# Performance work log

Hardware: AMD Instinct MI355X
Metric: run time of the kernel (lower is better)

The kernel has to match this reference:

```python
import jax, jax.numpy as jnp
import numpy as np

B, XD, PD, D, H = 512, 32768, 512, 64, 128  # batch, x_dim, proj_dim, latent_dim, per_dim_hidden
G1 = 1024  # gene projector hidden (hardcoded in module)


def _init(k, shape, fan_in):
    s = 1.0 / np.sqrt(fan_in)
    return jax.random.uniform(k, shape, jnp.float32, -s, s)


def setup_inputs() -> dict:
    key = jax.random.key(0)
    ks = jax.random.split(key, 16)
    return {
        "x": jax.random.normal(ks[0], (B, XD), jnp.float32),
        "z": jax.random.normal(ks[1], (B, D), jnp.float32),
        "perm": jax.random.permutation(ks[2], B).astype(jnp.int32),
        # shared gene projector
        "Wg1": _init(ks[3], (XD, G1), XD), "bg1": _init(ks[4], (G1,), XD),
        "Wg2": _init(ks[5], (G1, PD), G1), "bg2": _init(ks[6], (PD,), G1),
        # per-dimension 3-layer MLPs, stacked over D. Layer-1 weight [PD+1, H]
        # is split into the h-part Wh and the z-part Wz (last input column).
        "Wh": _init(ks[7], (D, PD, H), PD + 1),
        "Wz": _init(ks[8], (D, H), PD + 1),
        "b1": _init(ks[9], (D, H), PD + 1),
        "W2": _init(ks[10], (D, H, H), H), "b2": _init(ks[11], (D, H), H),
        "W3": _init(ks[12], (D, H), H), "b3": _init(ks[13], (D,), H),
    }


def reference(x, z, perm, Wg1, bg1, Wg2, bg2, Wh, Wz, b1, W2, b2, W3, b3):
    elu = jax.nn.elu
    # shared gene projector (eval mode: dropout = identity, no noise)
    h = elu(elu(x @ Wg1 + bg1) @ Wg2 + bg2)            # [B, PD]
    # batched layer-1 of all D per-dim nets; h-projection computed once and
    # reused for the marginal pass via permutation (h_shuffled = h[perm]).
    hWh = jnp.einsum('bp,dph->bdh', h, Wh)             # [B, D, H]
    zWz = z[:, :, None] * Wz[None]                     # [B, D, H]

    def head(a1_pre):
        a1 = elu(a1_pre)                               # [B, D, H]
        a2 = elu(jnp.einsum('bdh,dhk->bdk', a1, W2) + b2)
        return jnp.einsum('bdh,dh->bd', a2, W3) + b3   # [B, D] scalar scores

    joint_score = head(hWh + zWz + b1)                 # T(h, z_j)
    marg_score = head(hWh[perm] + zWz + b1)            # T(h_shuffled, z_j)

    emas = jnp.ones((D,), x.dtype)                     # buffer init = ones, eval: no update
    et = jnp.mean(jnp.exp(marg_score), axis=0)         # [D]
    mi = jnp.mean(joint_score, axis=0) - jnp.log(et / emas)
    return -jnp.mean(mi)
```

## Files before the change

kernel.cpp:

```cpp
#include <hip/hip_runtime.h>
#include <hip/hip_bf16.h>
#include <math.h>

#define B_  512
#define XD_ 32768
#define PD_ 512
#define D_  64
#define H_  128
#define G1_ 1024

typedef __attribute__((ext_vector_type(8))) short short8v;
typedef __attribute__((ext_vector_type(4))) float floatx4;

__device__ __forceinline__ float eluf(float v) { return v > 0.f ? v : expm1f(v); }

__device__ __forceinline__ void split8t(const float* c, short8v& h, short8v& l) {
    unsigned hu[8], lu[8];
    #pragma unroll
    for (int j = 0; j < 8; j++) {
        unsigned u = __float_as_uint(c[j]);
        hu[j] = u & 0xFFFF0000u;
        float res = c[j] - __uint_as_float(hu[j]);
        lu[j] = __float_as_uint(res);
    }
    uint4 hp, lp;
    hp.x = __builtin_amdgcn_perm(hu[1], hu[0], 0x07060302u);
    hp.y = __builtin_amdgcn_perm(hu[3], hu[2], 0x07060302u);
    hp.z = __builtin_amdgcn_perm(hu[5], hu[4], 0x07060302u);
    hp.w = __builtin_amdgcn_perm(hu[7], hu[6], 0x07060302u);
    lp.x = __builtin_amdgcn_perm(lu[1], lu[0], 0x07060302u);
    lp.y = __builtin_amdgcn_perm(lu[3], lu[2], 0x07060302u);
    lp.z = __builtin_amdgcn_perm(lu[5], lu[4], 0x07060302u);
    lp.w = __builtin_amdgcn_perm(lu[7], lu[6], 0x07060302u);
    h = __builtin_bit_cast(short8v, hp);
    l = __builtin_bit_cast(short8v, lp);
}

__global__ __launch_bounds__(256) void k_trs(const float* __restrict__ x,
                                             ushort* __restrict__ xh,
                                             ushort* __restrict__ xl) {
    const int k0 = blockIdx.x * 64;
    const int m0 = blockIdx.y * 64;
    const int t = threadIdx.x;
    const int m = t & 63;
    const int kq = t >> 6;
    #pragma unroll
    for (int i = 0; i < 2; i++) {
        int kg = kq * 2 + i;
        const float* p = x + (size_t)(m0 + m) * XD_ + k0 + kg * 8;
        float4 v0 = *(const float4*)p, v1 = *(const float4*)(p + 4);
        float c[8] = {v0.x, v0.y, v0.z, v0.w, v1.x, v1.y, v1.z, v1.w};
        short8v h, l; split8t(c, h, l);
        size_t off = ((size_t)((k0 >> 3) + kg) * B_ + m0 + m) * 8;
        *(short8v*)(xh + off) = h;
        *(short8v*)(xl + off) = l;
    }
}

__global__ __launch_bounds__(256, 2) void k_gemm1t(const ushort* __restrict__ xh,
                                                   const ushort* __restrict__ xl,
                                                   const float* __restrict__ Wg1,
                                                   float* __restrict__ part,
                                                   int KS) {
    __shared__ ushort Ah[2][4 * 128 * 8], Al[2][4 * 128 * 8];
    __shared__ ushort Bh[2][4 * 128 * 8], Bl[2][4 * 128 * 8];
    const int nt = blockIdx.x, mt = blockIdx.y, ks = blockIdx.z;
    const int t = threadIdx.x;
    const int w = t >> 6, lane = t & 63;
    const int q = lane >> 4, l15 = lane & 15;
    const int wr = w >> 1, wc = w & 1;
    const int q4 = t >> 6, pr = t & 63;
    const int k0 = ks * KS;

    const size_t aoff = (((size_t)(k0 >> 3) + q4) * B_ + mt * 128 + pr) * 8;
    const ushort* Agh = xh + aoff;
    const ushort* Agl = xl + aoff;
    const float*  Bg  = Wg1 + (size_t)(k0 + q4 * 8) * G1_ + nt * 128 + pr * 2;

    floatx4 acc[4][4];
    #pragma unroll
    for (int i = 0; i < 4; i++)
        #pragma unroll
        for (int j = 0; j < 4; j++) acc[i][j] = (floatx4){0.f, 0.f, 0.f, 0.f};

    uint4 pAh0, pAh1, pAl0, pAl1;
    float2 pb[8];

    auto loadT = [&](int kt) {
        size_t o = (size_t)kt * B_;
        pAh0 = *(const uint4*)(Agh + o);
        pAh1 = *(const uint4*)(Agh + o + 512);
        pAl0 = *(const uint4*)(Agl + o);
        pAl1 = *(const uint4*)(Agl + o + 512);
        const float* p = Bg + (size_t)kt * G1_;
        #pragma unroll
        for (int kk = 0; kk < 8; kk++) pb[kk] = *(const float2*)(p + (size_t)kk * G1_);
    };

    auto stage = [&](int buf) {
        float c0[8], c1[8];
        #pragma unroll
        for (int kk = 0; kk < 8; kk++) { c0[kk] = pb[kk].x; c1[kk] = pb[kk].y; }
        short8v bh0, bl0, bh1, bl1;
        split8t(c0, bh0, bl0); split8t(c1, bh1, bl1);
        int n0 = pr * 2;
        int i0 = (q4 * 128 + (n0 ^ q4)) * 8;
        int i1 = (q4 * 128 + ((n0 + 1) ^ q4)) * 8;
        *(short8v*)&Bh[buf][i0] = bh0; *(short8v*)&Bl[buf][i0] = bl0;
        *(short8v*)&Bh[buf][i1] = bh1; *(short8v*)&Bl[buf][i1] = bl1;
        int ia0 = (q4 * 128 + (pr ^ q4)) * 8;
        *(uint4*)&Ah[buf][ia0] = pAh0;
        *(uint4*)&Al[buf][ia0] = pAl0;
        *(uint4*)&Ah[buf][ia0 + 512] = pAh1;
        *(uint4*)&Al[buf][ia0 + 512] = pAl1;
    };

    auto mma = [&](int buf) {
        short8v af[4], alf[4], bf[4], blf[4];
        #pragma unroll
        for (int i = 0; i < 4; i++) {
            int m = wr * 64 + i * 16 + l15;
            int idx = (q * 128 + (m ^ q)) * 8;
            af[i]  = *(const short8v*)&Ah[buf][idx];
            alf[i] = *(const short8v*)&Al[buf][idx];
        }
        #pragma unroll
        for (int j = 0; j < 4; j++) {
            int n = wc * 64 + j * 16 + l15;
            int idx = (q * 128 + (n ^ q)) * 8;
            bf[j]  = *(const short8v*)&Bh[buf][idx];
            blf[j] = *(const short8v*)&Bl[buf][idx];
        }
        #pragma unroll
        for (int i = 0; i < 4; i++)
            #pragma unroll
            for (int j = 0; j < 4; j++) {
                acc[i][j] = __builtin_amdgcn_mfma_f32_16x16x32_bf16(af[i],  bf[j],  acc[i][j], 0, 0, 0);
                acc[i][j] = __builtin_amdgcn_mfma_f32_16x16x32_bf16(af[i],  blf[j], acc[i][j], 0, 0, 0);
                acc[i][j] = __builtin_amdgcn_mfma_f32_16x16x32_bf16(alf[i], bf[j],  acc[i][j], 0, 0, 0);
            }
    };

    loadT(0);
    stage(0);
    loadT(32);
    asm volatile("s_waitcnt lgkmcnt(0)" ::: "memory");
    __builtin_amdgcn_s_barrier();

    const int NT = KS >> 5;
    for (int it = 0; it < NT - 1; it++) {
        const int cur = it & 1;
        stage(cur ^ 1);
        if (it + 2 < NT) loadT((it + 2) * 32);
        mma(cur);
        asm volatile("s_waitcnt lgkmcnt(0)" ::: "memory");
        __builtin_amdgcn_s_barrier();
    }
    mma((NT - 1) & 1);

    float* P = part + (size_t)ks * (B_ * G1_) + (size_t)(mt * 128) * G1_ + nt * 128;
    #pragma unroll
    for (int i = 0; i < 4; i++)
        #pragma unroll
        for (int j = 0; j < 4; j++) {
            int col = wc * 64 + j * 16 + l15;
            #pragma unroll
            for (int r = 0; r < 4; r++) {
                int row = wr * 64 + i * 16 + q * 4 + r;
                P[(size_t)row * G1_ + col] = acc[i][j][r];
            }
        }
}

__global__ __launch_bounds__(256, 2) void k_gemm1m(const float* __restrict__ x,
                                                   const float* __restrict__ Wg1,
                                                   float* __restrict__ part,
                                                   int KS) {
    __shared__ ushort Ah[4 * 128 * 8], Al[4 * 128 * 8];
    __shared__ ushort Bh[4 * 128 * 8], Bl[4 * 128 * 8];
    const int nt = blockIdx.x, mt = blockIdx.y, ks = blockIdx.z;
    const int t = threadIdx.x;
    const int w = t >> 6, lane = t & 63;
    const int q = lane >> 4, l15 = lane & 15;
    const int wr = w >> 1, wc = w & 1;
    const int kbB = t >> 6, nb = t & 63;
    const int mA = t & 127, kbA = t >> 7;
    const int k0 = ks * KS;

    const float* Ag = x + (size_t)(mt * 128 + mA) * XD_ + k0 + kbA * 8;
    const float* Bg = Wg1 + (size_t)(k0 + kbB * 8) * G1_ + nt * 128 + nb * 2;

    floatx4 acc[4][4];
    #pragma unroll
    for (int i = 0; i < 4; i++)
        #pragma unroll
        for (int j = 0; j < 4; j++) acc[i][j] = (floatx4){0.f, 0.f, 0.f, 0.f};

    float4 pa0 = *(const float4*)(Ag);
    float4 pa1 = *(const float4*)(Ag + 4);
    float4 pa2 = *(const float4*)(Ag + 16);
    float4 pa3 = *(const float4*)(Ag + 20);
    float2 pb[8];
    #pragma unroll
    for (int kk = 0; kk < 8; kk++) pb[kk] = *(const float2*)(Bg + (size_t)kk * G1_);

    for (int kt = 0; kt < KS; kt += 32) {
        float cA0[8] = {pa0.x, pa0.y, pa0.z, pa0.w, pa1.x, pa1.y, pa1.z, pa1.w};
        float cA1[8] = {pa2.x, pa2.y, pa2.z, pa2.w, pa3.x, pa3.y, pa3.z, pa3.w};
        float c0[8], c1[8];
        #pragma unroll
        for (int kk = 0; kk < 8; kk++) { c0[kk] = pb[kk].x; c1[kk] = pb[kk].y; }
        short8v ah0, al0, ah1, al1, bh0, bl0, bh1, bl1;
        split8t(cA0, ah0, al0);
        split8t(cA1, ah1, al1);
        split8t(c0, bh0, bl0);
        split8t(c1, bh1, bl1);
        if (kt + 32 < KS) {
            pa0 = *(const float4*)(Ag + kt + 32);
            pa1 = *(const float4*)(Ag + kt + 36);
            pa2 = *(const float4*)(Ag + kt + 48);
            pa3 = *(const float4*)(Ag + kt + 52);
            const float* p = Bg + (size_t)(kt + 32) * G1_;
            #pragma unroll
            for (int kk = 0; kk < 8; kk++) pb[kk] = *(const float2*)(p + (size_t)kk * G1_);
        }
        {
            int ia0 = (kbA * 128 + (mA ^ kbA)) * 8;
            int ia1 = ((kbA + 2) * 128 + (mA ^ (kbA + 2))) * 8;
            *(short8v*)&Ah[ia0] = ah0; *(short8v*)&Al[ia0] = al0;
            *(short8v*)&Ah[ia1] = ah1; *(short8v*)&Al[ia1] = al1;
            int n0i = nb * 2;
            int i0 = (kbB * 128 + (n0i ^ kbB)) * 8;
            int i1 = (kbB * 128 + ((n0i + 1) ^ kbB)) * 8;
            *(short8v*)&Bh[i0] = bh0; *(short8v*)&Bl[i0] = bl0;
            *(short8v*)&Bh[i1] = bh1; *(short8v*)&Bl[i1] = bl1;
        }
        __syncthreads();
        short8v af[4], alf[4], bf[4], blf[4];
        #pragma unroll
        for (int i = 0; i < 4; i++) {
            int m = wr * 64 + i * 16 + l15;
            int idx = (q * 128 + (m ^ q)) * 8;
            af[i]  = *(const short8v*)&Ah[idx];
            alf[i] = *(const short8v*)&Al[idx];
        }
        #pragma unroll
        for (int j = 0; j < 4; j++) {
            int n = wc * 64 + j * 16 + l15;
            int idx = (q * 128 + (n ^ q)) * 8;
            bf[j]  = *(const short8v*)&Bh[idx];
            blf[j] = *(const short8v*)&Bl[idx];
        }
        #pragma unroll
        for (int i = 0; i < 4; i++)
            #pragma unroll
            for (int j = 0; j < 4; j++) {
                acc[i][j] = __builtin_amdgcn_mfma_f32_16x16x32_bf16(af[i],  bf[j],  acc[i][j], 0, 0, 0);
                acc[i][j] = __builtin_amdgcn_mfma_f32_16x16x32_bf16(af[i],  blf[j], acc[i][j], 0, 0, 0);
                acc[i][j] = __builtin_amdgcn_mfma_f32_16x16x32_bf16(alf[i], bf[j],  acc[i][j], 0, 0, 0);
            }
        __syncthreads();
    }
    float* P = part + (size_t)ks * (B_ * G1_) + (size_t)(mt * 128) * G1_ + nt * 128;
    #pragma unroll
    for (int i = 0; i < 4; i++)
        #pragma unroll
        for (int j = 0; j < 4; j++) {
            int col = wc * 64 + j * 16 + l15;
            #pragma unroll
            for (int r = 0; r < 4; r++) {
                int row = wr * 64 + i * 16 + q * 4 + r;
                P[(size_t)row * G1_ + col] = acc[i][j][r];
            }
        }
}

__global__ __launch_bounds__(256) void k_red1(const float* __restrict__ part,
                                              const float* __restrict__ bg1,
                                              ushort* __restrict__ Gh,
                                              ushort* __restrict__ Gl,
                                              int nparts) {
    int idx = (blockIdx.x * 256 + threadIdx.x) * 8;
    const int S = B_ * G1_;
    float c[8] = {};
    for (int k = 0; k < nparts; k++) {
        const float* p = part + (size_t)k * S + idx;
        float4 v0 = *(const float4*)p, v1 = *(const float4*)(p + 4);
        c[0] += v0.x; c[1] += v0.y; c[2] += v0.z; c[3] += v0.w;
        c[4] += v1.x; c[5] += v1.y; c[6] += v1.z; c[7] += v1.w;
    }
    int cb = idx & (G1_ - 1);
    float4 b0 = *(const float4*)(bg1 + cb), b1v = *(const float4*)(bg1 + cb + 4);
    c[0] = eluf(c[0] + b0.x); c[1] = eluf(c[1] + b0.y);
    c[2] = eluf(c[2] + b0.z); c[3] = eluf(c[3] + b0.w);
    c[4] = eluf(c[4] + b1v.x); c[5] = eluf(c[5] + b1v.y);
    c[6] = eluf(c[6] + b1v.z); c[7] = eluf(c[7] + b1v.w);
    short8v h, l; split8t(c, h, l);
    *(short8v*)(Gh + idx) = h;
    *(short8v*)(Gl + idx) = l;
}

__global__ __launch_bounds__(256, 2) void k_gemm2m(const ushort* __restrict__ Gh,
                                                   const ushort* __restrict__ Gl,
                                                   const float* __restrict__ Wg2,
                                                   float* __restrict__ part2) {
    __shared__ ushort Ah[4 * 64 * 8], Al[4 * 64 * 8];
    __shared__ ushort Bh[4 * 64 * 8], Bl[4 * 64 * 8];
    const int nt = blockIdx.x, mt = blockIdx.y, ks = blockIdx.z;
    const int t = threadIdx.x;
    const int w = t >> 6, lane = t & 63;
    const int q = lane >> 4, l15 = lane & 15;
    const int kb = (t >> 4) & 3;
    const int rb = (t & 15) | (w << 4);
    const int k0 = ks * 128;

    const int cB = t & 63, g = t >> 6;

    floatx4 acc[4];
    #pragma unroll
    for (int i = 0; i < 4; i++) acc[i] = (floatx4){0.f, 0.f, 0.f, 0.f};

    for (int kt = 0; kt < 128; kt += 32) {
        {
            const ushort* pH = Gh + (size_t)(mt * 64 + rb) * G1_ + k0 + kt + kb * 8;
            const ushort* pL = Gl + (size_t)(mt * 64 + rb) * G1_ + k0 + kt + kb * 8;
            uint4 vh = *(const uint4*)pH;
            uint4 vl = *(const uint4*)pL;
            int idx = (kb * 64 + (rb ^ kb)) * 8;
            *(uint4*)&Ah[idx] = vh;
            *(uint4*)&Al[idx] = vl;
        }
        {
            float c[8];
            const float* p = Wg2 + (size_t)(k0 + kt + g * 8) * PD_ + nt * 64 + cB;
            #pragma unroll
            for (int kk = 0; kk < 8; kk++) c[kk] = p[(size_t)kk * PD_];
            short8v h, l; split8t(c, h, l);
            int idx = (g * 64 + (cB ^ g)) * 8;
            *(short8v*)&Bh[idx] = h;
            *(short8v*)&Bl[idx] = l;
        }
        __syncthreads();
        short8v af[4], alf[4], bf, blf;
        #pragma unroll
        for (int i = 0; i < 4; i++) {
            int m = i * 16 + l15;
            int idx = (q * 64 + (m ^ q)) * 8;
            af[i]  = *(const short8v*)&Ah[idx];
            alf[i] = *(const short8v*)&Al[idx];
        }
        {
            int n = w * 16 + l15;
            int idx = (q * 64 + (n ^ q)) * 8;
            bf  = *(const short8v*)&Bh[idx];
            blf = *(const short8v*)&Bl[idx];
        }
        #pragma unroll
        for (int i = 0; i < 4; i++) {
            acc[i] = __builtin_amdgcn_mfma_f32_16x16x32_bf16(af[i],  bf,  acc[i], 0, 0, 0);
            acc[i] = __builtin_amdgcn_mfma_f32_16x16x32_bf16(af[i],  blf, acc[i], 0, 0, 0);
            acc[i] = __builtin_amdgcn_mfma_f32_16x16x32_bf16(alf[i], bf,  acc[i], 0, 0, 0);
        }
        __syncthreads();
    }
    float* P = part2 + (size_t)ks * (B_ * PD_) + (size_t)(mt * 64) * PD_ + nt * 64;
    #pragma unroll
    for (int i = 0; i < 4; i++) {
        int col = w * 16 + l15;
        #pragma unroll
        for (int r = 0; r < 4; r++) {
            int row = i * 16 + q * 4 + r;
            P[(size_t)row * PD_ + col] = acc[i][r];
        }
    }
}

__global__ __launch_bounds__(256) void k_red2(const float* __restrict__ part2,
                                              const float* __restrict__ bg2,
                                              ushort* __restrict__ hh,
                                              ushort* __restrict__ hl) {
    int idx = (blockIdx.x * 256 + threadIdx.x) * 8;
    const int S = B_ * PD_;
    float c[8] = {};
    #pragma unroll
    for (int k = 0; k < 8; k++) {
        const float* p = part2 + (size_t)k * S + idx;
        float4 v0 = *(const float4*)p, v1 = *(const float4*)(p + 4);
        c[0] += v0.x; c[1] += v0.y; c[2] += v0.z; c[3] += v0.w;
        c[4] += v1.x; c[5] += v1.y; c[6] += v1.z; c[7] += v1.w;
    }
    int cb = idx & (PD_ - 1);
    float4 b0 = *(const float4*)(bg2 + cb), b1v = *(const float4*)(bg2 + cb + 4);
    c[0] = eluf(c[0] + b0.x); c[1] = eluf(c[1] + b0.y);
    c[2] = eluf(c[2] + b0.z); c[3] = eluf(c[3] + b0.w);
    c[4] = eluf(c[4] + b1v.x); c[5] = eluf(c[5] + b1v.y);
    c[6] = eluf(c[6] + b1v.z); c[7] = eluf(c[7] + b1v.w);
    short8v h, l; split8t(c, h, l);
    *(short8v*)(hh + idx) = h;
    *(short8v*)(hl + idx) = l;
}

__global__ __launch_bounds__(256, 2) void k_hwh_m(const ushort* __restrict__ hh,
                                                  const ushort* __restrict__ hl,
                                                  const float* __restrict__ Wh,
                                                  float* __restrict__ hWh) {
    __shared__ ushort Ah[4 * 64 * 8], Al[4 * 64 * 8];
    __shared__ ushort Bh[4 * 128 * 8], Bl[4 * 128 * 8];
    const int d = blockIdx.x, mt = blockIdx.y;
    const int t = threadIdx.x;
    const int w = t >> 6, lane = t & 63;
    const int q = lane >> 4, l15 = lane & 15;
    const int kb = (t >> 4) & 3;
    const int rb = (t & 15) | (w << 4);

    const ushort* AgH = hh + (size_t)(mt * 64 + rb) * PD_ + kb * 8;
    const ushort* AgL = hl + (size_t)(mt * 64 + rb) * PD_ + kb * 8;
    const float* Bg = Wh + (size_t)d * (PD_ * H_) + (size_t)(kb * 8) * H_ + rb * 2;

    floatx4 acc[4][2];
    #pragma unroll
    for (int i = 0; i < 4; i++)
        #pragma unroll
        for (int j = 0; j < 2; j++) acc[i][j] = (floatx4){0.f, 0.f, 0.f, 0.f};

    uint4 pah = *(const uint4*)(AgH);
    uint4 pal = *(const uint4*)(AgL);
    float2 pb[8];
    #pragma unroll
    for (int kk = 0; kk < 8; kk++) pb[kk] = *(const float2*)(Bg + (size_t)kk * H_);

    for (int kt = 0; kt < PD_; kt += 32) {
        float c0[8], c1[8];
        #pragma unroll
        for (int kk = 0; kk < 8; kk++) { c0[kk] = pb[kk].x; c1[kk] = pb[kk].y; }
        short8v bh0, bl0, bh1, bl1;
        split8t(c0, bh0, bl0);
        split8t(c1, bh1, bl1);
        uint4 ah = pah, al = pal;
        if (kt + 32 < PD_) {
            pah = *(const uint4*)(AgH + kt + 32);
            pal = *(const uint4*)(AgL + kt + 32);
            const float* p = Bg + (size_t)(kt + 32) * H_;
            #pragma unroll
            for (int kk = 0; kk < 8; kk++) pb[kk] = *(const float2*)(p + (size_t)kk * H_);
        }
        {
            int idx = (kb * 64 + (rb ^ kb)) * 8;
            *(uint4*)&Ah[idx] = ah;
            *(uint4*)&Al[idx] = al;
            int n0i = rb * 2;
            int i0 = (kb * 128 + (n0i ^ kb)) * 8;
            int i1 = (kb * 128 + ((n0i + 1) ^ kb)) * 8;
            *(short8v*)&Bh[i0] = bh0; *(short8v*)&Bl[i0] = bl0;
            *(short8v*)&Bh[i1] = bh1; *(short8v*)&Bl[i1] = bl1;
        }
        __syncthreads();
        short8v af[4], alf[4], bf[2], blf[2];
        #pragma unroll
        for (int i = 0; i < 4; i++) {
            int m = i * 16 + l15;
            int idx = (q * 64 + (m ^ q)) * 8;
            af[i]  = *(const short8v*)&Ah[idx];
            alf[i] = *(const short8v*)&Al[idx];
        }
        #pragma unroll
        for (int j = 0; j < 2; j++) {
            int n = w * 32 + j * 16 + l15;
            int idx = (q * 128 + (n ^ q)) * 8;
            bf[j]  = *(const short8v*)&Bh[idx];
            blf[j] = *(const short8v*)&Bl[idx];
        }
        #pragma unroll
        for (int i = 0; i < 4; i++)
            #pragma unroll
            for (int j = 0; j < 2; j++) {
                acc[i][j] = __builtin_amdgcn_mfma_f32_16x16x32_bf16(af[i],  bf[j],  acc[i][j], 0, 0, 0);
                acc[i][j] = __builtin_amdgcn_mfma_f32_16x16x32_bf16(af[i],  blf[j], acc[i][j], 0, 0, 0);
                acc[i][j] = __builtin_amdgcn_mfma_f32_16x16x32_bf16(alf[i], bf[j],  acc[i][j], 0, 0, 0);
            }
        __syncthreads();
    }
    #pragma unroll
    for (int i = 0; i < 4; i++)
        #pragma unroll
        for (int j = 0; j < 2; j++) {
            int col = w * 32 + j * 16 + l15;
            #pragma unroll
            for (int r = 0; r < 4; r++) {
                int row = i * 16 + q * 4 + r;
                int b = mt * 64 + row;
                hWh[(size_t)b * (D_ * H_) + d * H_ + col] = acc[i][j][r];
            }
        }
}

__global__ __launch_bounds__(256, 2) void k_heads(const float* __restrict__ hWh,
                                                  const float* __restrict__ z,
                                                  const int* __restrict__ perm,
                                                  const float* __restrict__ Wz,
                                                  const float* __restrict__ b1,
                                                  const float* __restrict__ W2,
                                                  const float* __restrict__ b2,
                                                  const float* __restrict__ W3,
                                                  const float* __restrict__ b3,
                                                  float* __restrict__ jpart,
                                                  float* __restrict__ epart) {
    const int chunk = blockIdx.x;
    const int d = blockIdx.y;
    const int pass = blockIdx.z;
    const int t = threadIdx.x;
    const int b0 = chunk * 64;
    __shared__ ushort A1h[16 * 64 * 8];
    __shared__ ushort A1l[16 * 64 * 8];
    __shared__ float  BS[4096];
    ushort* Bh = (ushort*)BS;
    ushort* Bl = Bh + 4096;
    float*  sred = BS;

    const int w = t >> 6, lane = t & 63;
    const int q = lane >> 4, l15 = lane & 15;
    const int kb = (t >> 4) & 3;
    const int rb = (t & 15) | (w << 4);

    const float* W2d = W2 + (size_t)d * H_ * H_;
    const float* Wzd = Wz + d * H_;
    const float* b1d = b1 + d * H_;
    const float* b2d = b2 + d * H_;
    const float* W3d = W3 + d * H_;

    {
        int i = t >> 2;
        int kt = t & 3;
        int h0 = kt * 32;
        int bb = b0 + i;
        int src = (pass == 0) ? bb : perm[bb];
        float zv = z[bb * D_ + d];
        const float* hrow = hWh + (size_t)src * (D_ * H_) + d * H_;
        #pragma unroll
        for (int kq = 0; kq < 4; kq++) {
            float c[8];
            int kbase = h0 + kq * 8;
            float4 v0 = *(const float4*)(hrow + kbase);
            float4 v1 = *(const float4*)(hrow + kbase + 4);
            float4 w0 = *(const float4*)(Wzd + kbase);
            float4 w1 = *(const float4*)(Wzd + kbase + 4);
            float4 x0 = *(const float4*)(b1d + kbase);
            float4 x1 = *(const float4*)(b1d + kbase + 4);
            c[0] = eluf(v0.x + zv * w0.x + x0.x);
            c[1] = eluf(v0.y + zv * w0.y + x0.y);
            c[2] = eluf(v0.z + zv * w0.z + x0.z);
            c[3] = eluf(v0.w + zv * w0.w + x0.w);
            c[4] = eluf(v1.x + zv * w1.x + x1.x);
            c[5] = eluf(v1.y + zv * w1.y + x1.y);
            c[6] = eluf(v1.z + zv * w1.z + x1.z);
            c[7] = eluf(v1.w + zv * w1.w + x1.w);
            short8v hv, lv; split8t(c, hv, lv);
            int idx = ((kt * 4 + kq) * 64 + (i ^ kq)) * 8;
            *(short8v*)&A1h[idx] = hv;
            *(short8v*)&A1l[idx] = lv;
        }
    }
    __syncthreads();
    floatx4 acc[4][2];
    #pragma unroll
    for (int i = 0; i < 4; i++)
        #pragma unroll
        for (int j = 0; j < 2; j++) acc[i][j] = (floatx4){0.f, 0.f, 0.f, 0.f};
    for (int kt2 = 0; kt2 < 4; kt2++) {
        {
            float c0[8], c1[8];
            const float* p = W2d + (size_t)(kt2 * 32 + kb * 8) * H_ + rb * 2;
            #pragma unroll
            for (int kk = 0; kk < 8; kk++) {
                float2 v = *(const float2*)(p + (size_t)kk * H_);
                c0[kk] = v.x; c1[kk] = v.y;
            }
            short8v h0v, l0v, h1v, l1v;
            split8t(c0, h0v, l0v);
            split8t(c1, h1v, l1v);
            int n0i = rb * 2;
            int i0 = (kb * 128 + (n0i ^ kb)) * 8;
            int i1 = (kb * 128 + ((n0i + 1) ^ kb)) * 8;
            *(short8v*)&Bh[i0] = h0v; *(short8v*)&Bl[i0] = l0v;
            *(short8v*)&Bh[i1] = h1v; *(short8v*)&Bl[i1] = l1v;
        }
        __syncthreads();
        short8v af[4], alf[4], bf[2], blf[2];
        #pragma unroll
        for (int i = 0; i < 4; i++) {
            int m = i * 16 + l15;
            int idx = ((kt2 * 4 + q) * 64 + (m ^ q)) * 8;
            af[i]  = *(const short8v*)&A1h[idx];
            alf[i] = *(const short8v*)&A1l[idx];
        }
        #pragma unroll
        for (int j = 0; j < 2; j++) {
            int n = w * 32 + j * 16 + l15;
            int idx = (q * 128 + (n ^ q)) * 8;
            bf[j]  = *(const short8v*)&Bh[idx];
            blf[j] = *(const short8v*)&Bl[idx];
        }
        #pragma unroll
        for (int i = 0; i < 4; i++)
            #pragma unroll
            for (int j = 0; j < 2; j++) {
                acc[i][j] = __builtin_amdgcn_mfma_f32_16x16x32_bf16(af[i],  bf[j],  acc[i][j], 0, 0, 0);
                acc[i][j] = __builtin_amdgcn_mfma_f32_16x16x32_bf16(af[i],  blf[j], acc[i][j], 0, 0, 0);
                acc[i][j] = __builtin_amdgcn_mfma_f32_16x16x32_bf16(alf[i], bf[j],  acc[i][j], 0, 0, 0);
            }
        __syncthreads();
    }
    #pragma unroll
    for (int i = 0; i < 4; i++) {
        #pragma unroll
        for (int r = 0; r < 4; r++) {
            int b = i * 16 + q * 4 + r;
            float s = 0.f;
            #pragma unroll
            for (int j = 0; j < 2; j++) {
                int col = w * 32 + j * 16 + l15;
                float a2v = eluf(acc[i][j][r] + b2d[col]);
                s = fmaf(a2v, W3d[col], s);
            }
            sred[b * 64 + w * 16 + l15] = s;
        }
    }
    __syncthreads();
    float val = 0.f;
    if (t < 64) {
        float s = b3[d];
        const float4* row = (const float4*)&sred[t * 64];
        #pragma unroll
        for (int c = 0; c < 16; c++) {
            float4 v = row[c];
            s += v.x + v.y + v.z + v.w;
        }
        val = (pass == 0) ? s : expf(s);
        #pragma unroll
        for (int off = 32; off > 0; off >>= 1)
            val += __shfl_down(val, off, 64);
    }
    if (t == 0) {
        if (pass == 0) jpart[d * 8 + chunk] = val;
        else           epart[d * 8 + chunk] = val;
    }
}

__global__ void k_final(const float* __restrict__ jpart,
                        const float* __restrict__ epart,
                        float* __restrict__ out) {
    int t = threadIdx.x;
    float mj = 0.f, me = 0.f;
    #pragma unroll
    for (int c = 0; c < 8; c++) { mj += jpart[t * 8 + c]; me += epart[t * 8 + c]; }
    mj *= (1.f / 512.f);
    me *= (1.f / 512.f);
    float mi = mj - logf(me);
    #pragma unroll
    for (int off = 32; off > 0; off >>= 1) mi += __shfl_down(mi, off, 64);
    if (t == 0) out[0] = -mi * (1.f / 64.f);
}

extern "C" void kernel_launch(void* const* d_in, const int* in_sizes, int n_in,
                              void* d_out, int out_size, void* d_ws, size_t ws_size,
                              hipStream_t stream) {
    const float* x   = (const float*)d_in[0];
    const float* z   = (const float*)d_in[1];
    const int*  perm = (const int*)d_in[2];
    const float* Wg1 = (const float*)d_in[3];
    const float* bg1 = (const float*)d_in[4];
    const float* Wg2 = (const float*)d_in[5];
    const float* bg2 = (const float*)d_in[6];
    const float* Wh  = (const float*)d_in[7];
    const float* Wz  = (const float*)d_in[8];
    const float* b1  = (const float*)d_in[9];
    const float* W2  = (const float*)d_in[10];
    const float* b2  = (const float*)d_in[11];
    const float* W3  = (const float*)d_in[12];
    const float* b3  = (const float*)d_in[13];
    float* out = (float*)d_out;

    char* base = (char*)d_ws;
    const size_t PART_SLICE = (size_t)B_ * G1_ * sizeof(float);

    const size_t NEW_NEED = 16 * PART_SLICE + 67108864ull + 2097152 + 1048576 + 4096;

    if (ws_size >= NEW_NEED) {
        float* part  = (float*)base;
        ushort* xh   = (ushort*)(base + 33554432);
        ushort* xl   = (ushort*)(base + 67108864);
        float* hWh   = (float*)base;
        float* part2 = (float*)(base + 16777216);
        ushort* Gh   = (ushort*)(base + 100663296);
        ushort* Gl   = Gh + 524288;
        ushort* hh   = (ushort*)(base + 102760448);
        ushort* hl   = hh + 262144;
        float* jpart = (float*)(base + 103809024);
        float* epart = jpart + 512;

        k_trs<<<dim3(512, 8), 256, 0, stream>>>(x, xh, xl);
        k_gemm1t<<<dim3(8, 4, 16), 256, 0, stream>>>(xh, xl, Wg1, part, XD_ / 16);
        k_red1<<<256, 256, 0, stream>>>(part, bg1, Gh, Gl, 16);
        k_gemm2m<<<dim3(8, 8, 8), 256, 0, stream>>>(Gh, Gl, Wg2, part2);
        k_red2<<<128, 256, 0, stream>>>(part2, bg2, hh, hl);
        k_hwh_m<<<dim3(64, 8), 256, 0, stream>>>(hh, hl, Wh, hWh);
        k_heads<<<dim3(8, 64, 2), 256, 0, stream>>>(hWh, z, perm, Wz, b1, W2, b2, W3, b3,
                                                    jpart, epart);
        k_final<<<1, 64, 0, stream>>>(jpart, epart, out);
    } else {
        int nks = (ws_size >= (size_t)32 * PART_SLICE + 3145728 + 4096) ? 32 : 16;
        const int KS = XD_ / nks;
        const size_t partBytes = (size_t)nks * PART_SLICE;

        float* part  = (float*)base;
        float* hWh   = (float*)base;
        float* part2 = (float*)(base + 16777216);
        ushort* Gh   = (ushort*)(base + partBytes);
        ushort* Gl   = Gh + 524288;
        ushort* hh   = (ushort*)(base + partBytes + 2097152);
        ushort* hl   = hh + 262144;
        float* jpart = (float*)(base + partBytes + 3145728);
        float* epart = jpart + 512;

        k_gemm1m<<<dim3(8, 4, nks), 256, 0, stream>>>(x, Wg1, part, KS);
        k_red1<<<256, 256, 0, stream>>>(part, bg1, Gh, Gl, nks);
        k_gemm2m<<<dim3(8, 8, 8), 256, 0, stream>>>(Gh, Gl, Wg2, part2);
        k_red2<<<128, 256, 0, stream>>>(part2, bg2, hh, hl);
        k_hwh_m<<<dim3(64, 8), 256, 0, stream>>>(hh, hl, Wh, hWh);
        k_heads<<<dim3(8, 64, 2), 256, 0, stream>>>(hWh, z, perm, Wz, b1, W2, b2, W3, b3,
                                                    jpart, epart);
        k_final<<<1, 64, 0, stream>>>(jpart, epart, out);
    }
}
```

Measured before the change: 427.8 us.

## Widen gemm1 to 512 threads with deeper K tile, fold head passes into one block

The main projector GEMM now runs 512-thread blocks that stage 64 K-elements per iteration, with 8 waves tiled 4x2 over a 128x128 output. It also halves the split-K count from 16 to 8, which reduces the partial-sum traffic that the reduction kernel must read, and raises MFMA issue priority with s_setprio. The heads kernel loops over the joint and marginal passes inside one block instead of launching a separate z-dimension per pass, so W2 staging and launch work are shared. The cost is fewer blocks in gemm1 (256 instead of 512), which may lower occupancy and latency hiding, and longer serial work per heads block.

After: 428.3 us. Within noise of the previous version (+0.1%).

```diff
diff --git a/kernel.cpp b/kernel.cpp
--- a/kernel.cpp
+++ b/kernel.cpp
@@ -57,42 +57,42 @@
     }
 }
 
-__global__ __launch_bounds__(256, 2) void k_gemm1t(const ushort* __restrict__ xh,
+__global__ __launch_bounds__(512, 2) void k_gemm1t(const ushort* __restrict__ xh,
                                                    const ushort* __restrict__ xl,
                                                    const float* __restrict__ Wg1,
                                                    float* __restrict__ part,
                                                    int KS) {
-    __shared__ ushort Ah[2][4 * 128 * 8], Al[2][4 * 128 * 8];
-    __shared__ ushort Bh[2][4 * 128 * 8], Bl[2][4 * 128 * 8];
+    __shared__ ushort Ah[2][8 * 128 * 8], Al[2][8 * 128 * 8];
+    __shared__ ushort Bh[2][8 * 128 * 8], Bl[2][8 * 128 * 8];
     const int nt = blockIdx.x, mt = blockIdx.y, ks = blockIdx.z;
     const int t = threadIdx.x;
     const int w = t >> 6, lane = t & 63;
     const int q = lane >> 4, l15 = lane & 15;
-    const int wr = w >> 1, wc = w & 1;
-    const int q4 = t >> 6, pr = t & 63;
+    const int wm = w & 3, wn = w >> 2;
+    const int kg = t >> 6, pr = t & 63;
     const int k0 = ks * KS;
 
-    const size_t aoff = (((size_t)(k0 >> 3) + q4) * B_ + mt * 128 + pr) * 8;
+    const size_t aoff = (((size_t)(k0 >> 3) + kg) * B_ + mt * 128 + pr) * 8;
     const ushort* Agh = xh + aoff;
     const ushort* Agl = xl + aoff;
-    const float*  Bg  = Wg1 + (size_t)(k0 + q4 * 8) * G1_ + nt * 128 + pr * 2;
-
-    floatx4 acc[4][4];
-    #pragma unroll
-    for (int i = 0; i < 4; i++)
+    const float*  Bg  = Wg1 + (size_t)(k0 + kg * 8) * G1_ + nt * 128 + pr * 2;
+
+    floatx4 acc[2][4];
+    #pragma unroll
+    for (int i = 0; i < 2; i++)
         #pragma unroll
         for (int j = 0; j < 4; j++) acc[i][j] = (floatx4){0.f, 0.f, 0.f, 0.f};
 
     uint4 pAh0, pAh1, pAl0, pAl1;
     float2 pb[8];
 
-    auto loadT = [&](int kt) {
-        size_t o = (size_t)kt * B_;
+    auto loadT = [&](int T) {
+        size_t o = (size_t)T * B_ * 64;
         pAh0 = *(const uint4*)(Agh + o);
         pAh1 = *(const uint4*)(Agh + o + 512);
         pAl0 = *(const uint4*)(Agl + o);
         pAl1 = *(const uint4*)(Agl + o + 512);
-        const float* p = Bg + (size_t)kt * G1_;
+        const float* p = Bg + (size_t)T * 64 * G1_;
         #pragma unroll
         for (int kk = 0; kk < 8; kk++) pb[kk] = *(const float2*)(p + (size_t)kk * G1_);
     };
@@ -104,54 +104,60 @@
         short8v bh0, bl0, bh1, bl1;
         split8t(c0, bh0, bl0); split8t(c1, bh1, bl1);
         int n0 = pr * 2;
-        int i0 = (q4 * 128 + (n0 ^ q4)) * 8;
-        int i1 = (q4 * 128 + ((n0 + 1) ^ q4)) * 8;
+        int i0 = (kg * 128 + (n0 ^ kg)) * 8;
+        int i1 = (kg * 128 + ((n0 + 1) ^ kg)) * 8;
         *(short8v*)&Bh[buf][i0] = bh0; *(short8v*)&Bl[buf][i0] = bl0;
         *(short8v*)&Bh[buf][i1] = bh1; *(short8v*)&Bl[buf][i1] = bl1;
-        int ia0 = (q4 * 128 + (pr ^ q4)) * 8;
-        *(uint4*)&Ah[buf][ia0] = pAh0;
-        *(uint4*)&Al[buf][ia0] = pAl0;
-        *(uint4*)&Ah[buf][ia0 + 512] = pAh1;
-        *(uint4*)&Al[buf][ia0 + 512] = pAl1;
+        int ia = (kg * 128 + (pr ^ kg)) * 8;
+        *(uint4*)&Ah[buf][ia] = pAh0;
+        *(uint4*)&Al[buf][ia] = pAl0;
+        *(uint4*)&Ah[buf][ia + 512] = pAh1;
+        *(uint4*)&Al[buf][ia + 512] = pAl1;
     };
 
     auto mma = [&](int buf) {
-        short8v af[4], alf[4], bf[4], blf[4];
-        #pragma unroll
-        for (int i = 0; i < 4; i++) {
-            int m = wr * 64 + i * 16 + l15;
-            int idx = (q * 128 + (m ^ q)) * 8;
-            af[i]  = *(const short8v*)&Ah[buf][idx];
-            alf[i] = *(const short8v*)&Al[buf][idx];
-        }
-        #pragma unroll
-        for (int j = 0; j < 4; j++) {
-            int n = wc * 64 + j * 16 + l15;
-            int idx = (q * 128 + (n ^ q)) * 8;
-            bf[j]  = *(const short8v*)&Bh[buf][idx];
-            blf[j] = *(const short8v*)&Bl[buf][idx];
-        }
-        #pragma unroll
-        for (int i = 0; i < 4; i++)
+        #pragma unroll
+        for (int s = 0; s < 2; s++) {
+            const int kgq = s * 4 + q;
+            short8v af[2], alf[2], bf[4], blf[4];
+            #pragma unroll
+            for (int i = 0; i < 2; i++) {
+                int m = wm * 32 + i * 16 + l15;
+                int idx = (kgq * 128 + (m ^ kgq)) * 8;
+                af[i]  = *(const short8v*)&Ah[buf][idx];
+                alf[i] = *(const short8v*)&Al[buf][idx];
+            }
             #pragma unroll
             for (int j = 0; j < 4; j++) {
-                acc[i][j] = __builtin_amdgcn_mfma_f32_16x16x32_bf16(af[i],  bf[j],  acc[i][j], 0, 0, 0);
-                acc[i][j] = __builtin_amdgcn_mfma_f32_16x16x32_bf16(af[i],  blf[j], acc[i][j], 0, 0, 0);
-                acc[i][j] = __builtin_amdgcn_mfma_f32_16x16x32_bf16(alf[i], bf[j],  acc[i][j], 0, 0, 0);
-            }
+                int n = wn * 64 + j * 16 + l15;
+                int idx = (kgq * 128 + (n ^ kgq)) * 8;
+                bf[j]  = *(const short8v*)&Bh[buf][idx];
+                blf[j] = *(const short8v*)&Bl[buf][idx];
+            }
+            __builtin_amdgcn_s_setprio(1);
+            #pragma unroll
+            for (int i = 0; i < 2; i++)
+                #pragma unroll
+                for (int j = 0; j < 4; j++) {
+                    acc[i][j] = __builtin_amdgcn_mfma_f32_16x16x32_bf16(af[i],  bf[j],  acc[i][j], 0, 0, 0);
+                    acc[i][j] = __builtin_amdgcn_mfma_f32_16x16x32_bf16(af[i],  blf[j], acc[i][j], 0, 0, 0);
+                    acc[i][j] = __builtin_amdgcn_mfma_f32_16x16x32_bf16(alf[i], bf[j],  acc[i][j], 0, 0, 0);
+                }
+            __builtin_amdgcn_s_setprio(0);
+        }
     };
 
     loadT(0);
     stage(0);
-    loadT(32);
+    loadT(1);
     asm volatile("s_waitcnt lgkmcnt(0)" ::: "memory");
     __builtin_amdgcn_s_barrier();
 
-    const int NT = KS >> 5;
+    const int NT = KS >> 6;
     for (int it = 0; it < NT - 1; it++) {
         const int cur = it & 1;
         stage(cur ^ 1);
-        if (it + 2 < NT) loadT((it + 2) * 32);
+        if (it + 2 < NT) loadT(it + 2);
         mma(cur);
         asm volatile("s_waitcnt lgkmcnt(0)" ::: "memory");
         __builtin_amdgcn_s_barrier();
@@ -160,13 +166,13 @@
 
     float* P = part + (size_t)ks * (B_ * G1_) + (size_t)(mt * 128) * G1_ + nt * 128;
     #pragma unroll
-    for (int i = 0; i < 4; i++)
+    for (int i = 0; i < 2; i++)
         #pragma unroll
         for (int j = 0; j < 4; j++) {
-            int col = wc * 64 + j * 16 + l15;
+            int col = wn * 64 + j * 16 + l15;
             #pragma unroll
             for (int r = 0; r < 4; r++) {
-                int row = wr * 64 + i * 16 + q * 4 + r;
+                int row = wm * 32 + i * 16 + q * 4 + r;
                 P[(size_t)row * G1_ + col] = acc[i][j][r];
             }
         }
@@ -507,7 +513,6 @@
                                                   float* __restrict__ epart) {
     const int chunk = blockIdx.x;
     const int d = blockIdx.y;
-    const int pass = blockIdx.z;
     const int t = threadIdx.x;
     const int b0 = chunk * 64;
     __shared__ ushort A1h[16 * 64 * 8];
@@ -528,121 +533,126 @@
     const float* b2d = b2 + d * H_;
     const float* W3d = W3 + d * H_;
 
-    {
-        int i = t >> 2;
-        int kt = t & 3;
-        int h0 = kt * 32;
-        int bb = b0 + i;
-        int src = (pass == 0) ? bb : perm[bb];
-        float zv = z[bb * D_ + d];
-        const float* hrow = hWh + (size_t)src * (D_ * H_) + d * H_;
-        #pragma unroll
-        for (int kq = 0; kq < 4; kq++) {
-            float c[8];
-            int kbase = h0 + kq * 8;
-            float4 v0 = *(const float4*)(hrow + kbase);
-            float4 v1 = *(const float4*)(hrow + kbase + 4);
-            float4 w0 = *(const float4*)(Wzd + kbase);
-            float4 w1 = *(const float4*)(Wzd + kbase + 4);
-            float4 x0 = *(const float4*)(b1d + kbase);
-            float4 x1 = *(const float4*)(b1d + kbase + 4);
-            c[0] = eluf(v0.x + zv * w0.x + x0.x);
-            c[1] = eluf(v0.y + zv * w0.y + x0.y);
-            c[2] = eluf(v0.z + zv * w0.z + x0.z);
-            c[3] = eluf(v0.w + zv * w0.w + x0.w);
-            c[4] = eluf(v1.x + zv * w1.x + x1.x);
-            c[5] = eluf(v1.y + zv * w1.y + x1.y);
-            c[6] = eluf(v1.z + zv * w1.z + x1.z);
-            c[7] = eluf(v1.w + zv * w1.w + x1.w);
-            short8v hv, lv; split8t(c, hv, lv);
-            int idx = ((kt * 4 + kq) * 64 + (i ^ kq)) * 8;
-            *(short8v*)&A1h[idx] = hv;
-            *(short8v*)&A1l[idx] = lv;
-        }
-    }
-    __syncthreads();
-    floatx4 acc[4][2];
-    #pragma unroll
-    for (int i = 0; i < 4; i++)
-        #pragma unroll
-        for (int j = 0; j < 2; j++) acc[i][j] = (floatx4){0.f, 0.f, 0.f, 0.f};
-    for (int kt2 = 0; kt2 < 4; kt2++) {
+    float result0 = 0.f, result1 = 0.f;
+    for (int pass = 0; pass < 2; pass++) {
         {
-            float c0[8], c1[8];
-            const float* p = W2d + (size_t)(kt2 * 32 + kb * 8) * H_ + rb * 2;
-            #pragma unroll
-            for (int kk = 0; kk < 8; kk++) {
-                float2 v = *(const float2*)(p + (size_t)kk * H_);
-                c0[kk] = v.x; c1[kk] = v.y;
-            }
-            short8v h0v, l0v, h1v, l1v;
-            split8t(c0, h0v, l0v);
-            split8t(c1, h1v, l1v);
-            int n0i = rb * 2;
-            int i0 = (kb * 128 + (n0i ^ kb)) * 8;
-            int i1 = (kb * 128 + ((n0i + 1) ^ kb)) * 8;
-            *(short8v*)&Bh[i0] = h0v; *(short8v*)&Bl[i0] = l0v;
-            *(short8v*)&Bh[i1] = h1v; *(short8v*)&Bl[i1] = l1v;
-        }
-        __syncthreads();
-        short8v af[4], alf[4], bf[2], blf[2];
+            int i = t >> 2;
+            int kt = t & 3;
+            int h0 = kt * 32;
+            int bb = b0 + i;
+            int src = (pass == 0) ? bb : perm[bb];
+            float zv = z[bb * D_ + d];
+            const float* hrow = hWh + (size_t)src * (D_ * H_) + d * H_;
+            #pragma unroll
+            for (int kq = 0; kq < 4; kq++) {
+                float c[8];
+                int kbase = h0 + kq * 8;
+                float4 v0 = *(const float4*)(hrow + kbase);
+                float4 v1 = *(const float4*)(hrow + kbase + 4);
+                float4 w0 = *(const float4*)(Wzd + kbase);
+                float4 w1 = *(const float4*)(Wzd + kbase + 4);
+                float4 x0 = *(const float4*)(b1d + kbase);
+                float4 x1 = *(const float4*)(b1d + kbase + 4);
+                c[0] = eluf(v0.x + zv * w0.x + x0.x);
+                c[1] = eluf(v0.y + zv * w0.y + x0.y);
+                c[2] = eluf(v0.z + zv * w0.z + x0.z);
+                c[3] = eluf(v0.w + zv * w0.w + x0.w);
+                c[4] = eluf(v1.x + zv * w1.x + x1.x);
+                c[5] = eluf(v1.y + zv * w1.y + x1.y);
+                c[6] = eluf(v1.z + zv * w1.z + x1.z);
+                c[7] = eluf(v1.w + zv * w1.w + x1.w);
+                short8v hv, lv; split8t(c, hv, lv);
+                int idx = ((kt * 4 + kq) * 64 + (i ^ kq)) * 8;
+                *(short8v*)&A1h[idx] = hv;
+                *(short8v*)&A1l[idx] = lv;
+            }
+        }
+        __syncthreads();
+        floatx4 acc[4][2];
+        #pragma unroll
+        for (int i = 0; i < 4; i++)
+            #pragma unroll
+            for (int j = 0; j < 2; j++) acc[i][j] = (floatx4){0.f, 0.f, 0.f, 0.f};
+        for (int kt2 = 0; kt2 < 4; kt2++) {
+            {
+                float c0[8], c1[8];
+                const float* p = W2d + (size_t)(kt2 * 32 + kb * 8) * H_ + rb * 2;
+                #pragma unroll
+                for (int kk = 0; kk < 8; kk++) {
+                    float2 v = *(const float2*)(p + (size_t)kk * H_);
+                    c0[kk] = v.x; c1[kk] = v.y;
+                }
+                short8v h0v, l0v, h1v, l1v;
+                split8t(c0, h0v, l0v);
+                split8t(c1, h1v, l1v);
+                int n0i = rb * 2;
+                int i0 = (kb * 128 + (n0i ^ kb)) * 8;
+                int i1 = (kb * 128 + ((n0i + 1) ^ kb)) * 8;
+                *(short8v*)&Bh[i0] = h0v; *(short8v*)&Bl[i0] = l0v;
+                *(short8v*)&Bh[i1] = h1v; *(short8v*)&Bl[i1] = l1v;
+            }
+            __syncthreads();
+            short8v af[4], alf[4], bf[2], blf[2];
+            #pragma unroll
+            for (int i = 0; i < 4; i++) {
+                int m = i * 16 + l15;
+                int idx = ((kt2 * 4 + q) * 64 + (m ^ q)) * 8;
+                af[i]  = *(const short8v*)&A1h[idx];
+                alf[i] = *(const short8v*)&A1l[idx];
+            }
+            #pragma unroll
+            for (int j = 0; j < 2; j++) {
+                int n = w * 32 + j * 16 + l15;
+                int idx = (q * 128 + (n ^ q)) * 8;
+                bf[j]  = *(const short8v*)&Bh[idx];
+                blf[j] = *(const short8v*)&Bl[idx];
+            }
+            #pragma unroll
+            for (int i = 0; i < 4; i++)
+                #pragma unroll
+                for (int j = 0; j < 2; j++) {
+                    acc[i][j] = __builtin_amdgcn_mfma_f32_16x16x32_bf16(af[i],  bf[j],  acc[i][j], 0, 0, 0);
+                    acc[i][j] = __builtin_amdgcn_mfma_f32_16x16x32_bf16(af[i],  blf[j], acc[i][j], 0, 0, 0);
+                    acc[i][j] = __builtin_amdgcn_mfma_f32_16x16x32_bf16(alf[i], bf[j],  acc[i][j], 0, 0, 0);
+                }
+            __syncthreads();
+        }
         #pragma unroll
         for (int i = 0; i < 4; i++) {
-            int m = i * 16 + l15;
-            int idx = ((kt2 * 4 + q) * 64 + (m ^ q)) * 8;
-            af[i]  = *(const short8v*)&A1h[idx];
-            alf[i] = *(const short8v*)&A1l[idx];
-        }
-        #pragma unroll
-        for (int j = 0; j < 2; j++) {
-            int n = w * 32 + j * 16 + l15;
-            int idx = (q * 128 + (n ^ q)) * 8;
-            bf[j]  = *(const short8v*)&Bh[idx];
-            blf[j] = *(const short8v*)&Bl[idx];
-        }
-        #pragma unroll
-        for (int i = 0; i < 4; i++)
-            #pragma unroll
-            for (int j = 0; j < 2; j++) {
-                acc[i][j] = __builtin_amdgcn_mfma_f32_16x16x32_bf16(af[i],  bf[j],  acc[i][j], 0, 0, 0);
-                acc[i][j] = __builtin_amdgcn_mfma_f32_16x16x32_bf16(af[i],  blf[j], acc[i][j], 0, 0, 0);
-                acc[i][j] = __builtin_amdgcn_mfma_f32_16x16x32_bf16(alf[i], bf[j],  acc[i][j], 0, 0, 0);
-            }
-        __syncthreads();
-    }
-    #pragma unroll
-    for (int i = 0; i < 4; i++) {
-        #pragma unroll
-        for (int r = 0; r < 4; r++) {
-            int b = i * 16 + q * 4 + r;
-            float s = 0.f;
-            #pragma unroll
-            for (int j = 0; j < 2; j++) {
-                int col = w * 32 + j * 16 + l15;
-                float a2v = eluf(acc[i][j][r] + b2d[col]);
-                s = fmaf(a2v, W3d[col], s);
-            }
-            sred[b * 64 + w * 16 + l15] = s;
-        }
-    }
-    __syncthreads();
-    float val = 0.f;
-    if (t < 64) {
-        float s = b3[d];
-        const float4* row = (const float4*)&sred[t * 64];
-        #pragma unroll
-        for (int c = 0; c < 16; c++) {
-            float4 v = row[c];
-            s += v.x + v.y + v.z + v.w;
-        }
-        val = (pass == 0) ? s : expf(s);
-        #pragma unroll
-        for (int off = 32; off > 0; off >>= 1)
-            val += __shfl_down(val, off, 64);
+            #pragma unroll
+            for (int r = 0; r < 4; r++) {
+                int b = i * 16 + q * 4 + r;
+                float s = 0.f;
+                #pragma unroll
+                for (int j = 0; j < 2; j++) {
+                    int col = w * 32 + j * 16 + l15;
+                    float a2v = eluf(acc[i][j][r] + b2d[col]);
+                    s = fmaf(a2v, W3d[col], s);
+                }
+                sred[b * 64 + w * 16 + l15] = s;
+            }
+        }
+        __syncthreads();
+        float val = 0.f;
+        if (t < 64) {
+            float s = b3[d];
+            const float4* row = (const float4*)&sred[t * 64];
+            #pragma unroll
+            for (int c = 0; c < 16; c++) {
+                float4 v = row[c];
+                s += v.x + v.y + v.z + v.w;
+            }
+            val = (pass == 0) ? s : expf(s);
+            #pragma unroll
+            for (int off = 32; off > 0; off >>= 1)
+                val += __shfl_down(val, off, 64);
+        }
+        if (t == 0) { if (pass == 0) result0 = val; else result1 = val; }
+        __syncthreads();
     }
     if (t == 0) {
-        if (pass == 0) jpart[d * 8 + chunk] = val;
-        else           epart[d * 8 + chunk] = val;
+        jpart[d * 8 + chunk] = result0;
+        epart[d * 8 + chunk] = result1;
     }
 }
 
@@ -699,13 +709,13 @@
         float* epart = jpart + 512;
 
         k_trs<<<dim3(512, 8), 256, 0, stream>>>(x, xh, xl);
-        k_gemm1t<<<dim3(8, 4, 16), 256, 0, stream>>>(xh, xl, Wg1, part, XD_ / 16);
-        k_red1<<<256, 256, 0, stream>>>(part, bg1, Gh, Gl, 16);
+        k_gemm1t<<<dim3(8, 4, 8), 512, 0, stream>>>(xh, xl, Wg1, part, XD_ / 8);
+        k_red1<<<256, 256, 0, stream>>>(part, bg1, Gh, Gl, 8);
         k_gemm2m<<<dim3(8, 8, 8), 256, 0, stream>>>(Gh, Gl, Wg2, part2);
         k_red2<<<128, 256, 0, stream>>>(part2, bg2, hh, hl);
         k_hwh_m<<<dim3(64, 8), 256, 0, stream>>>(hh, hl, Wh, hWh);
-        k_heads<<<dim3(8, 64, 2), 256, 0, stream>>>(hWh, z, perm, Wz, b1, W2, b2, W3, b3,
-                                                    jpart, epart);
+        k_heads<<<dim3(8, 64), 256, 0, stream>>>(hWh, z, perm, Wz, b1, W2, b2, W3, b3,
+                                                 jpart, epart);
         k_final<<<1, 64, 0, stream>>>(jpart, epart, out);
     } else {
         int nks = (ws_size >= (size_t)32 * PART_SLICE + 3145728 + 4096) ? 32 : 16;
@@ -727,8 +737,8 @@
         k_gemm2m<<<dim3(8, 8, 8), 256, 0, stream>>>(Gh, Gl, Wg2, part2);
         k_red2<<<128, 256, 0, stream>>>(part2, bg2, hh, hl);
         k_hwh_m<<<dim3(64, 8), 256, 0, stream>>>(hh, hl, Wh, hWh);
-        k_heads<<<dim3(8, 64, 2), 256, 0, stream>>>(hWh, z, perm, Wz, b1, W2, b2, W3, b3,
-                                                    jpart, epart);
+        k_heads<<<dim3(8, 64), 256, 0, stream>>>(hWh, z, perm, Wz, b1, W2, b2, W3, b3,
+                                                 jpart, epart);
         k_final<<<1, 64, 0, stream>>>(jpart, epart, out);
     }
 }
```
